# Kernel optimization log

Measured on AMD Instinct MI355X. Metric: run time of the kernel, lower is better.

The kernel has to match this reference:

```python
import jax, jax.numpy as jnp
import numpy as np

B, L, D_MODEL = 8, 2048, 512
D_STATE, EXPAND = 16, 2
D_INNER = D_MODEL * EXPAND
EPS = 1e-5


def setup_inputs() -> dict:
    key = jax.random.key(0)
    ks = jax.random.split(key, 16)
    s = 0.02
    return {
        "x": jax.random.normal(ks[0], (B, L, D_MODEL), jnp.float32),
        "norm_w": jnp.ones((D_MODEL,), jnp.float32),
        "norm_b": jnp.zeros((D_MODEL,), jnp.float32),
        "in_proj_w": jax.random.normal(ks[1], (2 * D_INNER, D_MODEL), jnp.float32) * s,
        "in_proj_b": jnp.zeros((2 * D_INNER,), jnp.float32),
        "conv_w": jax.random.normal(ks[2], (D_INNER, 1, 3), jnp.float32) * s,  # depthwise, groups=D_INNER
        "conv_b": jnp.zeros((D_INNER,), jnp.float32),
        "gru_w_ih": jax.random.normal(ks[3], (3 * D_STATE, D_INNER), jnp.float32) * s,
        "gru_w_hh": jax.random.normal(ks[4], (3 * D_STATE, D_STATE), jnp.float32) * s,
        "gru_b_ih": jnp.zeros((3 * D_STATE,), jnp.float32),
        "gru_b_hh": jnp.zeros((3 * D_STATE,), jnp.float32),
        "ssm_proj_w": jax.random.normal(ks[5], (D_INNER, D_STATE), jnp.float32) * s,
        "ssm_proj_b": jnp.zeros((D_INNER,), jnp.float32),
        "out_proj_w": jax.random.normal(ks[6], (D_MODEL, D_INNER), jnp.float32) * s,
        "out_proj_b": jnp.zeros((D_MODEL,), jnp.float32),
    }


def _silu(a):
    return a * jax.nn.sigmoid(a)


def reference(x, norm_w, norm_b, in_proj_w, in_proj_b, conv_w, conv_b,
              gru_w_ih, gru_w_hh, gru_b_ih, gru_b_hh,
              ssm_proj_w, ssm_proj_b, out_proj_w, out_proj_b):
    residual = x
    # LayerNorm over last dim
    mu = jnp.mean(x, axis=-1, keepdims=True)
    var = jnp.mean(jnp.square(x - mu), axis=-1, keepdims=True)
    xn = (x - mu) * jax.lax.rsqrt(var + EPS) * norm_w + norm_b
    # in_proj -> split into x_ and gate z
    xz = jnp.einsum("bld,ed->ble", xn, in_proj_w) + in_proj_b
    x_, z = jnp.split(xz, 2, axis=-1)  # each [B, L, D_INNER]
    # depthwise conv1d, kernel 3, pad 1
    xc = jax.lax.conv_general_dilated(
        x_.transpose(0, 2, 1), conv_w, window_strides=(1,), padding=[(1, 1)],
        dimension_numbers=("NCH", "OIH", "NCH"), feature_group_count=D_INNER)
    x_ = _silu((xc + conv_b[None, :, None]).transpose(0, 2, 1))  # [B, L, D_INNER]
    # GRU (batch_first), h0 = 0; PyTorch gate math
    xg = jnp.einsum("bld,gd->blg", x_, gru_w_ih) + gru_b_ih  # [B, L, 3H]
    def step(h, xt):
        gh = h @ gru_w_hh.T + gru_b_hh
        xr, xz_, xnn = jnp.split(xt, 3, axis=-1)
        hr, hz, hn = jnp.split(gh, 3, axis=-1)
        r = jax.nn.sigmoid(xr + hr)
        zt = jax.nn.sigmoid(xz_ + hz)
        n = jnp.tanh(xnn + r * hn)
        h_new = (1.0 - zt) * n + zt * h
        return h_new, h_new
    h0 = jnp.zeros((x.shape[0], D_STATE), x.dtype)
    _, ys = jax.lax.scan(step, h0, xg.transpose(1, 0, 2))
    y = ys.transpose(1, 0, 2)  # [B, L, D_STATE]
    y = jnp.einsum("bls,es->ble", y, ssm_proj_w) + ssm_proj_b
    y = y * _silu(z)
    y = jnp.einsum("ble,de->bld", y, out_proj_w) + out_proj_b
    return residual + y  # dropout = identity (eval mode)
```

## Files before the change

kernel.cpp:

```cpp
#include <hip/hip_runtime.h>
#include <hip/hip_bf16.h>

#define B_  8
#define L_  2048
#define DM  512
#define DI  1024
#define T_  (B_*L_)
#define EPSF 1e-5f
#define GCH 32

typedef short v8s __attribute__((ext_vector_type(8)));
typedef float v4f __attribute__((ext_vector_type(4)));
typedef float v2f __attribute__((ext_vector_type(2)));

__device__ __forceinline__ float bf2f(unsigned short h){
    union { unsigned int u; float f; } v; v.u = ((unsigned int)h) << 16; return v.f;
}
__device__ __forceinline__ unsigned short f2bf(float f){
    union { float f; unsigned int u; } v; v.f = f;
    unsigned int r = v.u + 0x7fffu + ((v.u >> 16) & 1u);
    return (unsigned short)(r >> 16);
}
__device__ __forceinline__ float sig_fast(float x){
    float e = __builtin_amdgcn_exp2f(x * -1.44269504089f);
    return __builtin_amdgcn_rcpf(1.f + e);
}
__device__ __forceinline__ float tanh_pade(float x){
    float t = x*x;
    float m = 27.f*x;
    float num = __builtin_fmaf(x, t, m);
    float den = __builtin_fmaf(9.f, t, 27.f);
    float v = num * __builtin_amdgcn_rcpf(den);
    return fminf(1.f, fmaxf(-1.f, v));
}
__device__ __forceinline__ float sig_pade(float x){
    return __builtin_fmaf(0.5f, tanh_pade(0.5f*x), 0.5f);
}
__device__ __forceinline__ v2f vfma2(v2f a, v2f b, v2f c){
#if __has_builtin(__builtin_elementwise_fma)
    return __builtin_elementwise_fma(a, b, c);
#else
    return (v2f){__builtin_fmaf(a.x,b.x,c.x), __builtin_fmaf(a.y,b.y,c.y)};
#endif
}

template<int CTRL>
__device__ __forceinline__ float dpp_rot(float x){
    int xi = __builtin_bit_cast(int, x);
    int r = __builtin_amdgcn_update_dpp(xi, xi, CTRL, 0xf, 0xf, false);
    return __builtin_bit_cast(float, r);
}

__device__ __forceinline__ void gload_lds16(const unsigned short* g, unsigned short* l){
    __builtin_amdgcn_global_load_lds(
        (const __attribute__((address_space(1))) unsigned int*)(const void*)g,
        (__attribute__((address_space(3))) unsigned int*)(void*)l,
        16, 0, 0);
}

#define WAITBAR_VM8()  do{ asm volatile("s_waitcnt vmcnt(8)\n\ts_barrier" ::: "memory"); __builtin_amdgcn_sched_barrier(0); }while(0)
#define WAITBAR_VM0()  do{ asm volatile("s_waitcnt vmcnt(0)\n\ts_barrier" ::: "memory"); __builtin_amdgcn_sched_barrier(0); }while(0)
#define BAR_ONLY()     do{ asm volatile("s_barrier" ::: "memory"); }while(0)

__global__ void cvt_all_kernel(const float* __restrict__ in_w, const float* __restrict__ out_w,
                               const float* __restrict__ gih_w,
                               unsigned short* __restrict__ in_wb, unsigned short* __restrict__ out_wb,
                               unsigned short* __restrict__ gih_wb){
    int i = (blockIdx.x*256 + threadIdx.x)*4;
    const float* src; unsigned short* dst; int off;
    if(i < 1048576){ src = in_w;  dst = in_wb;  off = i; }
    else if(i < 1572864){ src = out_w; dst = out_wb; off = i - 1048576; }
    else {
        off = i - 1572864;
        int row = off >> 10;
        unsigned int p0 = 0, p1 = 0;
        if(row < 48){
            float4 f = *reinterpret_cast<const float4*>(gih_w + off);
            p0 = f2bf(f.x) | ((unsigned int)f2bf(f.y)<<16);
            p1 = f2bf(f.z) | ((unsigned int)f2bf(f.w)<<16);
        }
        uint2 pk = {p0,p1};
        *reinterpret_cast<uint2*>(gih_wb + off) = pk;
        return;
    }
    float4 f = *reinterpret_cast<const float4*>(src + off);
    unsigned int p0 = f2bf(f.x) | ((unsigned int)f2bf(f.y)<<16);
    unsigned int p1 = f2bf(f.z) | ((unsigned int)f2bf(f.w)<<16);
    uint2 pk = {p0,p1};
    *reinterpret_cast<uint2*>(dst + off) = pk;
}

__global__ __launch_bounds__(256) void ln_kernel(
    const float* __restrict__ x, const float* __restrict__ w,
    const float* __restrict__ b, unsigned short* __restrict__ xn){
    int row = blockIdx.x*4 + (threadIdx.x >> 6);
    int lane = threadIdx.x & 63;
    const float* xr = x + (size_t)row*DM + lane*8;
    float4 v0 = *reinterpret_cast<const float4*>(xr);
    float4 v1 = *reinterpret_cast<const float4*>(xr + 4);
    float v[8] = {v0.x,v0.y,v0.z,v0.w,v1.x,v1.y,v1.z,v1.w};
    float s = 0.f, sq = 0.f;
    #pragma unroll
    for(int j=0;j<8;j++){ s += v[j]; sq += v[j]*v[j]; }
    #pragma unroll
    for(int o=32;o>0;o>>=1){ s += __shfl_xor(s,o); sq += __shfl_xor(sq,o); }
    float mu  = s*(1.f/DM);
    float var = sq*(1.f/DM) - mu*mu;
    float rs  = rsqrtf(var + EPSF);
    int c = lane*8;
    float4 w0 = *reinterpret_cast<const float4*>(w + c);
    float4 w1 = *reinterpret_cast<const float4*>(w + c + 4);
    float4 b0 = *reinterpret_cast<const float4*>(b + c);
    float4 b1 = *reinterpret_cast<const float4*>(b + c + 4);
    float wv[8] = {w0.x,w0.y,w0.z,w0.w,w1.x,w1.y,w1.z,w1.w};
    float bv[8] = {b0.x,b0.y,b0.z,b0.w,b1.x,b1.y,b1.z,b1.w};
    unsigned short o8[8];
    #pragma unroll
    for(int j=0;j<8;j++) o8[j] = f2bf((v[j]-mu)*rs*wv[j] + bv[j]);
    uint4 pk;
    pk.x = o8[0] | ((unsigned int)o8[1]<<16);
    pk.y = o8[2] | ((unsigned int)o8[3]<<16);
    pk.z = o8[4] | ((unsigned int)o8[5]<<16);
    pk.w = o8[6] | ((unsigned int)o8[7]<<16);
    *reinterpret_cast<uint4*>(xn + (size_t)row*DM + c) = pk;
}

template<int OUTMODE>
__global__ __launch_bounds__(256) void gemm_mfma(
    const unsigned short* __restrict__ A, int lda,
    const unsigned short* __restrict__ Bw, int K,
    const float* __restrict__ bias,
    const float* __restrict__ resid,
    void* __restrict__ Cout, int ldc)
{
    __shared__ __align__(16) unsigned short As[2][128][64];
    __shared__ __align__(16) unsigned short Bs[2][128][64];
    const int nwg = gridDim.x*gridDim.y;
    const int idx = blockIdx.y*gridDim.x + blockIdx.x;
    const int q8  = nwg >> 3;
    const int swz = (idx & 7)*q8 + (idx >> 3);
    const int m0 = (swz / gridDim.x) * 128;
    const int n0 = (swz % gridDim.x) * 128;
    const int tid = threadIdx.x;
    const int wave = tid >> 6;
    const int lane = tid & 63;
    const int wm = (wave >> 1) * 64, wn = (wave & 1) * 64;
    const int r16 = lane & 15, kc = lane >> 4;
    const int lrow = lane >> 3;
    const int lcs  = (((lane & 7) ^ lrow) << 3);
    const int rsw  = (r16 & 7) << 3;

    v4f acc[4][4];
    #pragma unroll
    for(int i=0;i<4;i++)
        #pragma unroll
        for(int j=0;j<4;j++) acc[i][j] = (v4f){0.f,0.f,0.f,0.f};

    const int nk = K >> 6;
    #define STAGE(k0_, bsel_) {                                                   \
        _Pragma("unroll")                                                         \
        for(int c=0;c<4;c++){                                                     \
            int chunk = wave*4 + c;                                               \
            int row = chunk*8 + lrow;                                             \
            gload_lds16(A  + (size_t)(m0+row)*lda + (k0_) + lcs, &As[bsel_][chunk*8][0]); \
            gload_lds16(Bw + (size_t)(n0+row)*K   + (k0_) + lcs, &Bs[bsel_][chunk*8][0]); \
        }                                                                         \
    }
    #define COMPUTE(bsel_) {                                                      \
        _Pragma("unroll")                                                         \
        for(int kk=0;kk<2;kk++){                                                  \
            v8s af[4], bfr[4];                                                    \
            _Pragma("unroll")                                                     \
            for(int i=0;i<4;i++)                                                  \
                af[i] = *reinterpret_cast<const v8s*>(&As[bsel_][wm + i*16 + r16][(kk*32 + kc*8) ^ rsw]); \
            _Pragma("unroll")                                                     \
            for(int j=0;j<4;j++)                                                  \
                bfr[j] = *reinterpret_cast<const v8s*>(&Bs[bsel_][wn + j*16 + r16][(kk*32 + kc*8) ^ rsw]); \
            _Pragma("unroll")                                                     \
            for(int i=0;i<4;i++)                                                  \
                _Pragma("unroll")                                                 \
                for(int j=0;j<4;j++)                                              \
                    acc[i][j] = __builtin_amdgcn_mfma_f32_16x16x32_bf16(bfr[j], af[i], acc[i][j], 0, 0, 0); \
        }                                                                         \
    }

    STAGE(0, 0);
    STAGE(64, 1);
    for(int ki=0; ki<nk-1; ki++){
        WAITBAR_VM8();
        COMPUTE(ki & 1);
        BAR_ONLY();
        if(ki+2 < nk) STAGE((ki+2)*64, ki & 1);
    }
    WAITBAR_VM0();
    COMPUTE((nk-1) & 1);

    float4 bias4[4];
    #pragma unroll
    for(int j=0;j<4;j++)
        bias4[j] = *reinterpret_cast<const float4*>(bias + n0 + wn + j*16 + kc*4);

    #pragma unroll
    for(int i=0;i<4;i++){
        size_t row = (size_t)(m0 + wm + i*16 + r16);
        #pragma unroll
        for(int j=0;j<4;j++){
            int c4 = n0 + wn + j*16 + kc*4;
            float4 b4 = bias4[j];
            float v0 = acc[i][j][0] + b4.x;
            float v1 = acc[i][j][1] + b4.y;
            float v2 = acc[i][j][2] + b4.z;
            float v3 = acc[i][j][3] + b4.w;
            if(OUTMODE == 0){
                unsigned int p0 = f2bf(v0) | ((unsigned int)f2bf(v1)<<16);
                unsigned int p1 = f2bf(v2) | ((unsigned int)f2bf(v3)<<16);
                uint2 pk = {p0, p1};
                *reinterpret_cast<uint2*>((unsigned short*)Cout + row*ldc + c4) = pk;
            } else {
                float4 rv = *reinterpret_cast<const float4*>(resid + row*ldc + c4);
                float4 ov = {v0+rv.x, v1+rv.y, v2+rv.z, v3+rv.w};
                *reinterpret_cast<float4*>((float*)Cout + row*ldc + c4) = ov;
            }
        }
    }
    #undef STAGE
    #undef COMPUTE
}

__global__ __launch_bounds__(256) void gemm_xg(
    const unsigned short* __restrict__ xz,
    const float* __restrict__ cw, const float* __restrict__ cb,
    const unsigned short* __restrict__ Bw,
    const float* __restrict__ bias,
    float* __restrict__ xgT)
{
    __shared__ __align__(16) unsigned short As[64][72];
    __shared__ __align__(16) unsigned short Bs[64][72];
    const int m0 = blockIdx.x * 64;
    const int tid = threadIdx.x;
    const int wave = tid >> 6;
    const int lane = tid & 63;
    const int wm = (wave >> 1) * 32, wn = (wave & 1) * 32;
    const int r16 = lane & 15, kc = lane >> 4;
    const int srow = tid >> 3;
    const int scol = (tid & 7) * 8;

    v4f acc[2][2];
    #pragma unroll
    for(int i=0;i<2;i++){ acc[i][0] = (v4f){0,0,0,0}; acc[i][1] = (v4f){0,0,0,0}; }

    for(int k0=0;k0<1024;k0+=64){
        const int c = k0 + scol;
        float w0[8], w1[8], w2[8], cb8[8];
        #pragma unroll
        for(int j=0;j<8;j++){
            w0[j] = cw[(c+j)*3+0]; w1[j] = cw[(c+j)*3+1]; w2[j] = cw[(c+j)*3+2];
            cb8[j] = cb[c+j];
        }
        #pragma unroll
        for(int p=0;p<2;p++){
            int rr = srow + p*32;
            int t = m0 + rr;
            int ll = t & (L_-1);
            const unsigned short* rowp = xz + (size_t)t*2048 + c;
            uint4 uc = *reinterpret_cast<const uint4*>(rowp);
            uint4 up = {0,0,0,0}, un = {0,0,0,0};
            if(ll > 0)      up = *reinterpret_cast<const uint4*>(rowp - 2048);
            if(ll < L_-1)   un = *reinterpret_cast<const uint4*>(rowp + 2048);
            unsigned int ucw[4] = {uc.x,uc.y,uc.z,uc.w};
            unsigned int upw[4] = {up.x,up.y,up.z,up.w};
            unsigned int unw[4] = {un.x,un.y,un.z,un.w};
            unsigned short o8[8];
            #pragma unroll
            for(int j=0;j<8;j++){
                float curv = bf2f((unsigned short)((ucw[j>>1] >> ((j&1)*16)) & 0xffffu));
                float prvv = bf2f((unsigned short)((upw[j>>1] >> ((j&1)*16)) & 0xffffu));
                float nxtv = bf2f((unsigned short)((unw[j>>1] >> ((j&1)*16)) & 0xffffu));
                float v = __builtin_fmaf(w0[j], prvv, __builtin_fmaf(w1[j], curv, __builtin_fmaf(w2[j], nxtv, cb8[j])));
                o8[j] = f2bf(v * sig_fast(v));
            }
            uint4 pk;
            pk.x = o8[0] | ((unsigned int)o8[1]<<16);
            pk.y = o8[2] | ((unsigned int)o8[3]<<16);
            pk.z = o8[4] | ((unsigned int)o8[5]<<16);
            pk.w = o8[6] | ((unsigned int)o8[7]<<16);
            *reinterpret_cast<uint4*>(&As[rr][scol]) = pk;
        }
        #pragma unroll
        for(int p=0;p<2;p++){
            int rr = srow + p*32;
            uint4 bv = *reinterpret_cast<const uint4*>(Bw + (size_t)rr*1024 + k0 + scol);
            *reinterpret_cast<uint4*>(&Bs[rr][scol]) = bv;
        }
        __syncthreads();
        #pragma unroll
        for(int kk=0;kk<2;kk++){
            v8s af[2], bfr[2];
            #pragma unroll
            for(int i=0;i<2;i++)
                af[i] = *reinterpret_cast<const v8s*>(&As[wm + i*16 + r16][kk*32 + kc*8]);
            #pragma unroll
            for(int j=0;j<2;j++)
                bfr[j] = *reinterpret_cast<const v8s*>(&Bs[wn + j*16 + r16][kk*32 + kc*8]);
            #pragma unroll
            for(int i=0;i<2;i++)
                #pragma unroll
                for(int j=0;j<2;j++)
                    acc[i][j] = __builtin_amdgcn_mfma_f32_16x16x32_bf16(af[i], bfr[j], acc[i][j], 0, 0, 0);
        }
        __syncthreads();
    }
    #pragma unroll
    for(int j=0;j<2;j++){
        int col = wn + j*16 + r16;
        if(col < 48){
            float bj = bias[col];
            #pragma unroll
            for(int i=0;i<2;i++){
                int rowb = m0 + wm + i*16 + kc*4;
                int bb = rowb >> 11, ll = rowb & 2047;
                float4 v4 = {acc[i][j][0]+bj, acc[i][j][1]+bj, acc[i][j][2]+bj, acc[i][j][3]+bj};
                *reinterpret_cast<float4*>(xgT + ((size_t)bb*48 + col)*2048 + ll) = v4;
            }
        }
    }
}

__global__ __launch_bounds__(64) void gru_kernel(
    const float* __restrict__ xgT, const float* __restrict__ whh,
    const float* __restrict__ bhh, float* __restrict__ yT){
    __shared__ __align__(16) float ystage[4][16][36];
    const int tid = threadIdx.x;
    const int s = tid & 15;
    const int sl = tid >> 4;
    const int scan = blockIdx.x*4 + sl;
    const int c = scan >> 3;
    const int b = scan & 7;
    const int warm_groups = (c == 0) ? 0 : 12;
    const int ngroups = warm_groups + 8;
    const int tload = c*GCH - warm_groups*4;

    int mk = __builtin_amdgcn_update_dpp(s, s, 0x121, 0xf, 0xf, false);
    int dir = (mk == ((s+15)&15)) ? 15 : 1;

    v2f w2r[8], w2z[8], w2n[8];
    #pragma unroll
    for(int k=0;k<8;k++){
        int jA = (s + k*dir) & 15;
        int jB = (s + (k+8)*dir) & 15;
        w2r[k] = (v2f){ whh[(     s)*16 + jA], whh[(     s)*16 + jB] };
        w2z[k] = (v2f){ whh[(16 + s)*16 + jA], whh[(16 + s)*16 + jB] };
        w2n[k] = (v2f){ whh[(32 + s)*16 + jA], whh[(32 + s)*16 + jB] };
    }
    const float br = bhh[s], bz = bhh[16+s], bn = bhh[32+s];
    const float* xr_ = xgT + ((size_t)b*48 +      s)*L_ + tload;
    const float* xz_ = xgT + ((size_t)b*48 + 16 + s)*L_ + tload;
    const float* xn_ = xgT + ((size_t)b*48 + 32 + s)*L_ + tload;

    union F4 { float4 v; float a[4]; };
    F4 fr[4], fz[4], fn[4];
    #pragma unroll
    for(int g=0; g<4; g++){
        fr[g].v = *reinterpret_cast<const float4*>(xr_ + g*4);
        fz[g].v = *reinterpret_cast<const float4*>(xz_ + g*4);
        fn[g].v = *reinterpret_cast<const float4*>(xn_ + g*4);
        fr[g].a[0]+=br; fr[g].a[1]+=br; fr[g].a[2]+=br; fr[g].a[3]+=br;
        fz[g].a[0]+=bz; fz[g].a[1]+=bz; fz[g].a[2]+=bz; fz[g].a[3]+=bz;
    }
    v2f h2[8];
    #pragma unroll
    for(int k=0;k<8;k++) h2[k] = (v2f){0.f, 0.f};

    for(int G=0; G<ngroups; ++G){
        int qq = G & 3;
        int nx = G + 4; if(nx > ngroups-1) nx = ngroups-1;
        float4 pr = *reinterpret_cast<const float4*>(xr_ + nx*4);
        float4 pz = *reinterpret_cast<const float4*>(xz_ + nx*4);
        float4 pn = *reinterpret_cast<const float4*>(xn_ + nx*4);
        F4 ho;
        #pragma unroll
        for(int j=0;j<4;j++){
            v2f ar0 = w2r[0]*h2[0], ar1 = w2r[1]*h2[1], ar2 = w2r[2]*h2[2], ar3 = w2r[3]*h2[3];
            v2f az0 = w2z[0]*h2[0], az1 = w2z[1]*h2[1], az2 = w2z[2]*h2[2], az3 = w2z[3]*h2[3];
            v2f an0 = w2n[0]*h2[0], an1 = w2n[1]*h2[1], an2 = w2n[2]*h2[2], an3 = w2n[3]*h2[3];
            ar0 = vfma2(w2r[4],h2[4],ar0); ar1 = vfma2(w2r[5],h2[5],ar1);
            ar2 = vfma2(w2r[6],h2[6],ar2); ar3 = vfma2(w2r[7],h2[7],ar3);
            az0 = vfma2(w2z[4],h2[4],az0); az1 = vfma2(w2z[5],h2[5],az1);
            az2 = vfma2(w2z[6],h2[6],az2); az3 = vfma2(w2z[7],h2[7],az3);
            an0 = vfma2(w2n[4],h2[4],an0); an1 = vfma2(w2n[5],h2[5],an1);
            an2 = vfma2(w2n[6],h2[6],an2); an3 = vfma2(w2n[7],h2[7],an3);
            v2f arp = (ar0+ar1)+(ar2+ar3);
            v2f azp = (az0+az1)+(az2+az3);
            v2f anp = (an0+an1)+(an2+an3);
            float gr = arp.x + arp.y;
            float gz = azp.x + azp.y;
            float gn = anp.x + anp.y;
            float r   = sig_pade(fr[qq].a[j] + gr);
            float zt  = sig_pade(fz[qq].a[j] + gz);
            float pre = __builtin_fmaf(r, bn + gn, fn[qq].a[j]);
            float n   = tanh_pade(pre);
            float h0  = h2[0].x;
            float hnew = __builtin_fmaf(zt, h0 - n, n);
            ho.a[j] = hnew;
            h2[0] = (v2f){ hnew,                 dpp_rot<0x128>(hnew) };
            h2[1] = (v2f){ dpp_rot<0x121>(hnew), dpp_rot<0x129>(hnew) };
            h2[2] = (v2f){ dpp_rot<0x122>(hnew), dpp_rot<0x12A>(hnew) };
            h2[3] = (v2f){ dpp_rot<0x123>(hnew), dpp_rot<0x12B>(hnew) };
            h2[4] = (v2f){ dpp_rot<0x124>(hnew), dpp_rot<0x12C>(hnew) };
            h2[5] = (v2f){ dpp_rot<0x125>(hnew), dpp_rot<0x12D>(hnew) };
            h2[6] = (v2f){ dpp_rot<0x126>(hnew), dpp_rot<0x12E>(hnew) };
            h2[7] = (v2f){ dpp_rot<0x127>(hnew), dpp_rot<0x12F>(hnew) };
        }
        if(G >= warm_groups){
            *reinterpret_cast<float4*>(&ystage[sl][s][(G - warm_groups)*4]) = ho.v;
        }
        pr.x+=br; pr.y+=br; pr.z+=br; pr.w+=br;
        pz.x+=bz; pz.y+=bz; pz.z+=bz; pz.w+=bz;
        fr[qq].v = pr; fz[qq].v = pz; fn[qq].v = pn;
    }
    __syncthreads();
    #pragma unroll
    for(int k=0;k<8;k++){
        int slot = tid + k*64;
        int row = slot >> 3, c4 = slot & 7;
        int fsl = row >> 4, fs = row & 15;
        int fscan = blockIdx.x*4 + fsl;
        int fc = fscan >> 3, fb = fscan & 7;
        float4 v = *reinterpret_cast<const float4*>(&ystage[0][0][0] + (size_t)row*36 + c4*4);
        *reinterpret_cast<float4*>(yT + ((size_t)fb*16 + fs)*L_ + fc*GCH + c4*4) = v;
    }
}

__global__ __launch_bounds__(256) void gated_kernel(
    const float* __restrict__ yT, const float* __restrict__ sw,
    const float* __restrict__ sb, unsigned short* __restrict__ xz){
    const int tid = threadIdx.x;
    const int e = tid * 4;
    float w[4][16]; float sb4[4];
    #pragma unroll
    for(int j=0;j<4;j++){
        sb4[j] = sb[e+j];
        float4 a0 = *reinterpret_cast<const float4*>(sw + (size_t)(e+j)*16);
        float4 a1 = *reinterpret_cast<const float4*>(sw + (size_t)(e+j)*16 + 4);
        float4 a2 = *reinterpret_cast<const float4*>(sw + (size_t)(e+j)*16 + 8);
        float4 a3 = *reinterpret_cast<const float4*>(sw + (size_t)(e+j)*16 + 12);
        w[j][0]=a0.x; w[j][1]=a0.y; w[j][2]=a0.z; w[j][3]=a0.w;
        w[j][4]=a1.x; w[j][5]=a1.y; w[j][6]=a1.z; w[j][7]=a1.w;
        w[j][8]=a2.x; w[j][9]=a2.y; w[j][10]=a2.z; w[j][11]=a2.w;
        w[j][12]=a3.x; w[j][13]=a3.y; w[j][14]=a3.z; w[j][15]=a3.w;
    }
    for(int t = blockIdx.x; t < T_; t += gridDim.x){
        const int bb = t >> 11, ll = t & 2047;
        float yv[16];
        #pragma unroll
        for(int k=0;k<16;k++) yv[k] = yT[((size_t)bb*16 + k)*L_ + ll];
        uint2 zz = *reinterpret_cast<const uint2*>(xz + (size_t)t*2048 + 1024 + e);
        float zv[4] = {bf2f(zz.x&0xffffu), bf2f(zz.x>>16), bf2f(zz.y&0xffffu), bf2f(zz.y>>16)};
        unsigned short o[4];
        #pragma unroll
        for(int j=0;j<4;j++){
            float a0=sb4[j], a1=0.f, a2=0.f, a3=0.f;
            #pragma unroll
            for(int k=0;k<16;k+=4){
                a0 = __builtin_fmaf(w[j][k  ], yv[k  ], a0);
                a1 = __builtin_fmaf(w[j][k+1], yv[k+1], a1);
                a2 = __builtin_fmaf(w[j][k+2], yv[k+2], a2);
                a3 = __builtin_fmaf(w[j][k+3], yv[k+3], a3);
            }
            float a = (a0+a1)+(a2+a3);
            float sz = zv[j]*sig_fast(zv[j]);
            o[j] = f2bf(a*sz);
        }
        unsigned int p0 = o[0] | ((unsigned int)o[1]<<16);
        unsigned int p1 = o[2] | ((unsigned int)o[3]<<16);
        uint2 pk = {p0,p1};
        *reinterpret_cast<uint2*>(xz + (size_t)t*2048 + e) = pk;
    }
}

extern "C" void kernel_launch(void* const* d_in, const int* in_sizes, int n_in,
                              void* d_out, int out_size, void* d_ws, size_t ws_size,
                              hipStream_t stream) {
    const float* x        = (const float*)d_in[0];
    const float* norm_w   = (const float*)d_in[1];
    const float* norm_b   = (const float*)d_in[2];
    const float* in_w     = (const float*)d_in[3];
    const float* in_b     = (const float*)d_in[4];
    const float* conv_w   = (const float*)d_in[5];
    const float* conv_b   = (const float*)d_in[6];
    const float* gih_w    = (const float*)d_in[7];
    const float* ghh_w    = (const float*)d_in[8];
    const float* gih_b    = (const float*)d_in[9];
    const float* ghh_b    = (const float*)d_in[10];
    const float* ssm_w    = (const float*)d_in[11];
    const float* ssm_b    = (const float*)d_in[12];
    const float* out_w    = (const float*)d_in[13];
    const float* out_b    = (const float*)d_in[14];
    float* out = (float*)d_out;

    char* w = (char*)d_ws;
    unsigned short* xn    = (unsigned short*)(w);
    unsigned short* xz    = (unsigned short*)(w + 16777216);
    float*          xg    = (float*)(w + 117440512);
    float*          yb    = (float*)(w + 120586240);
    unsigned short* in_wb = (unsigned short*)(w + 121634816);
    unsigned short* out_wb= (unsigned short*)(w + 123731968);
    unsigned short* gih_wb= (unsigned short*)(w + 124780544);

    cvt_all_kernel<<<1600, 256, 0, stream>>>(in_w, out_w, gih_w, in_wb, out_wb, gih_wb);
    ln_kernel<<<T_/4, 256, 0, stream>>>(x, norm_w, norm_b, xn);
    gemm_mfma<0><<<dim3(2048/128, T_/128), 256, 0, stream>>>(xn, DM, in_wb, DM, in_b, nullptr, xz, 2*DI);
    gemm_xg<<<T_/64, 256, 0, stream>>>(xz, conv_w, conv_b, gih_wb, gih_b, xg);
    gru_kernel<<<128, 64, 0, stream>>>(xg, ghh_w, ghh_b, yb);
    gated_kernel<<<1024, 256, 0, stream>>>(yb, ssm_w, ssm_b, xz);
    gemm_mfma<2><<<dim3(DM/128, T_/128), 256, 0, stream>>>(xz, 2*DI, out_wb, DI, out_b, x, out, DM);
}
```

Before: 176.0 us.

## Enlarge GEMM tile to 256x128 with 8 waves and triple-buffered LDS

The two MFMA GEMMs now use 256-row by 128-column tiles computed by 512 threads (8 waves), and the LDS pipeline grows from double to triple buffering with adjusted vmcnt waits. MFMA blocks are also wrapped in s_setprio to favour matrix issue. The aim is more B-tile reuse per load and deeper latency hiding. In exchange LDS use rises to about 144 KB per block, which lowers occupancy and halves the grid size, so wave-level parallelism may suffer.

```diff
diff --git a/kernel.cpp b/kernel.cpp
--- a/kernel.cpp
+++ b/kernel.cpp
@@ -58,8 +58,7 @@
         16, 0, 0);
 }
 
-#define WAITBAR_VM8()  do{ asm volatile("s_waitcnt vmcnt(8)\n\ts_barrier" ::: "memory"); __builtin_amdgcn_sched_barrier(0); }while(0)
-#define WAITBAR_VM0()  do{ asm volatile("s_waitcnt vmcnt(0)\n\ts_barrier" ::: "memory"); __builtin_amdgcn_sched_barrier(0); }while(0)
+#define WAITBAR(N_)    do{ asm volatile("s_waitcnt vmcnt(" #N_ ")\n\ts_barrier" ::: "memory"); __builtin_amdgcn_sched_barrier(0); }while(0)
 #define BAR_ONLY()     do{ asm volatile("s_barrier" ::: "memory"); }while(0)
 
 __global__ void cvt_all_kernel(const float* __restrict__ in_w, const float* __restrict__ out_w,
@@ -126,25 +125,26 @@
 }
 
 template<int OUTMODE>
-__global__ __launch_bounds__(256) void gemm_mfma(
+__global__ __launch_bounds__(512) void gemm_mfma(
     const unsigned short* __restrict__ A, int lda,
     const unsigned short* __restrict__ Bw, int K,
     const float* __restrict__ bias,
     const float* __restrict__ resid,
     void* __restrict__ Cout, int ldc)
 {
-    __shared__ __align__(16) unsigned short As[2][128][64];
-    __shared__ __align__(16) unsigned short Bs[2][128][64];
+    __shared__ __align__(16) unsigned short As[3][256][64];
+    __shared__ __align__(16) unsigned short Bs[3][128][64];
     const int nwg = gridDim.x*gridDim.y;
     const int idx = blockIdx.y*gridDim.x + blockIdx.x;
     const int q8  = nwg >> 3;
     const int swz = (idx & 7)*q8 + (idx >> 3);
-    const int m0 = (swz / gridDim.x) * 128;
+    const int m0 = (swz / gridDim.x) * 256;
     const int n0 = (swz % gridDim.x) * 128;
     const int tid = threadIdx.x;
     const int wave = tid >> 6;
     const int lane = tid & 63;
-    const int wm = (wave >> 1) * 64, wn = (wave & 1) * 64;
+    const int wm = (wave >> 1) * 64;
+    const int wn = (wave & 1) * 64;
     const int r16 = lane & 15, kc = lane >> 4;
     const int lrow = lane >> 3;
     const int lcs  = (((lane & 7) ^ lrow) << 3);
@@ -159,11 +159,14 @@
     const int nk = K >> 6;
     #define STAGE(k0_, bsel_) {                                                   \
         _Pragma("unroll")                                                         \
-        for(int c=0;c<4;c++){                                                     \
-            int chunk = wave*4 + c;                                               \
-            int row = chunk*8 + lrow;                                             \
-            gload_lds16(A  + (size_t)(m0+row)*lda + (k0_) + lcs, &As[bsel_][chunk*8][0]); \
-            gload_lds16(Bw + (size_t)(n0+row)*K   + (k0_) + lcs, &Bs[bsel_][chunk*8][0]); \
+        for(int p=0;p<4;p++){                                                     \
+            int row = p*64 + wave*8;                                              \
+            gload_lds16(A + (size_t)(m0+row+lrow)*lda + (k0_) + lcs, &As[bsel_][row][0]); \
+        }                                                                         \
+        _Pragma("unroll")                                                         \
+        for(int p=0;p<2;p++){                                                     \
+            int row = p*64 + wave*8;                                              \
+            gload_lds16(Bw + (size_t)(n0+row+lrow)*K + (k0_) + lcs, &Bs[bsel_][row][0]); \
         }                                                                         \
     }
     #define COMPUTE(bsel_) {                                                      \
@@ -176,24 +179,29 @@
             _Pragma("unroll")                                                     \
             for(int j=0;j<4;j++)                                                  \
                 bfr[j] = *reinterpret_cast<const v8s*>(&Bs[bsel_][wn + j*16 + r16][(kk*32 + kc*8) ^ rsw]); \
+            __builtin_amdgcn_s_setprio(1);                                        \
             _Pragma("unroll")                                                     \
             for(int i=0;i<4;i++)                                                  \
                 _Pragma("unroll")                                                 \
                 for(int j=0;j<4;j++)                                              \
                     acc[i][j] = __builtin_amdgcn_mfma_f32_16x16x32_bf16(bfr[j], af[i], acc[i][j], 0, 0, 0); \
+            __builtin_amdgcn_s_setprio(0);                                        \
         }                                                                         \
     }
 
-    STAGE(0, 0);
-    STAGE(64, 1);
-    for(int ki=0; ki<nk-1; ki++){
-        WAITBAR_VM8();
-        COMPUTE(ki & 1);
+    STAGE(0,   0);
+    STAGE(64,  1);
+    STAGE(128, 2);
+    int ki = 0;
+    for(; ki < nk-3; ki++){
+        WAITBAR(12);
+        COMPUTE(ki % 3);
         BAR_ONLY();
-        if(ki+2 < nk) STAGE((ki+2)*64, ki & 1);
-    }
-    WAITBAR_VM0();
-    COMPUTE((nk-1) & 1);
+        STAGE((ki+3)*64, ki % 3);
+    }
+    WAITBAR(12); COMPUTE((nk-3) % 3); BAR_ONLY();
+    WAITBAR(6);  COMPUTE((nk-2) % 3); BAR_ONLY();
+    WAITBAR(0);  COMPUTE((nk-1) % 3);
 
     float4 bias4[4];
     #pragma unroll
@@ -509,9 +517,9 @@
 
     cvt_all_kernel<<<1600, 256, 0, stream>>>(in_w, out_w, gih_w, in_wb, out_wb, gih_wb);
     ln_kernel<<<T_/4, 256, 0, stream>>>(x, norm_w, norm_b, xn);
-    gemm_mfma<0><<<dim3(2048/128, T_/128), 256, 0, stream>>>(xn, DM, in_wb, DM, in_b, nullptr, xz, 2*DI);
+    gemm_mfma<0><<<dim3(2048/128, T_/256), 512, 0, stream>>>(xn, DM, in_wb, DM, in_b, nullptr, xz, 2*DI);
     gemm_xg<<<T_/64, 256, 0, stream>>>(xz, conv_w, conv_b, gih_wb, gih_b, xg);
     gru_kernel<<<128, 64, 0, stream>>>(xg, ghh_w, ghh_b, yb);
     gated_kernel<<<1024, 256, 0, stream>>>(yb, ssm_w, ssm_b, xz);
-    gemm_mfma<2><<<dim3(DM/128, T_/128), 256, 0, stream>>>(xz, 2*DI, out_wb, DI, out_b, x, out, DM);
-}
+    gemm_mfma<2><<<dim3(DM/128, T_/256), 512, 0, stream>>>(xz, 2*DI, out_wb, DI, out_b, x, out, DM);
+}
```

Result: slower. 186.4 us (+5.9%).
